# Kernel tuning notes

Hardware: AMD Instinct MI355X
Metric: run time of the kernel (lower is better)

The kernel has to match this reference:

```python
import jax, jax.numpy as jnp
import numpy as np

B, S, D_IN, D_EMB = 16, 8192, 256, 256
LEVELS = 8  # pywt default max level for db1 with signal length 256: log2(256)
INV_SQRT2 = np.float32(1.0 / np.sqrt(2.0))


def haar_wavedec_concat(x, levels):
    """Multi-level Haar (db1) DWT along last axis; returns coeffs concatenated
    in pywt order [cA_L, cD_L, ..., cD_1]. Assumes last dim = 2**levels,
    so 'symmetric' padding is a no-op (filter length 2, even lengths).
    pywt db1 convention: cA[k]=(x[2k]+x[2k+1])/sqrt2, cD[k]=(x[2k]-x[2k+1])/sqrt2.
    """
    details = []
    a = x
    for _ in range(levels):
        even = a[..., ::2]
        odd = a[..., 1::2]
        details.append((even - odd) * INV_SQRT2)
        a = (even + odd) * INV_SQRT2
    return jnp.concatenate([a] + details[::-1], axis=-1)


def setup_inputs() -> dict:
    key = jax.random.key(0)
    k_x, k_w, k_b = jax.random.split(key, 3)
    x = jax.random.normal(k_x, (B, S, D_IN), dtype=jnp.float32)
    # nn.Linear(input_dim, embed_dim): W is (embed_dim, input_dim)
    bound = np.float32(1.0 / np.sqrt(D_IN))
    W = jax.random.uniform(k_w, (D_EMB, D_IN), dtype=jnp.float32, minval=-bound, maxval=bound)
    b = jax.random.uniform(k_b, (D_EMB,), dtype=jnp.float32, minval=-bound, maxval=bound)
    return {"x": x, "W": W, "b": b}


def reference(x, W, b):
    coeffs = haar_wavedec_concat(x, LEVELS)  # (B, S, D_IN)
    # concatenated coeff length == D_IN exactly, so no pad/trim (matches original no-op branch)
    return jnp.einsum('bsd,ed->bse', coeffs, W) + b
```

## Files before the change

### kernel.cpp

```cpp
#include <hip/hip_runtime.h>
#include <hip/hip_bf16.h>

typedef short short8 __attribute__((ext_vector_type(8)));
typedef float f32x4 __attribute__((ext_vector_type(4)));

#define INV_SQRT2F 0.70710678118654752440f

__device__ __forceinline__ unsigned short f2bf(float f) {
  union { float f; unsigned u; } v; v.f = f;
  unsigned u = v.u;
  unsigned r = (u + 0x7FFFu + ((u >> 16) & 1u)) >> 16;
  return (unsigned short)r;
}

__global__ void haar_pack(const float* __restrict__ W, unsigned short* __restrict__ Wp) {
  __shared__ float cbuf[4][256];
  __shared__ float buf0[4][256];
  __shared__ float buf1[4][256];
  const int tid = threadIdx.x;
  const int w = tid >> 6, l = tid & 63;
  const int e = blockIdx.x * 4 + w;
  const float* row = W + e * 256;
  for (int k = l; k < 256; k += 64) cbuf[w][k] = row[k];
  __syncthreads();
  if (l == 0) buf0[w][0] = cbuf[w][0];
  __syncthreads();
  float* A = buf0[w];
  float* Bv = buf1[w];
  int len = 1;
  for (int s = 0; s < 8; ++s) {
    for (int k = l; k < len; k += 64) {
      float av = A[k], dv = cbuf[w][len + k];
      Bv[2 * k]     = (av + dv) * INV_SQRT2F;
      Bv[2 * k + 1] = (av - dv) * INV_SQRT2F;
    }
    __syncthreads();
    float* t = A; A = Bv; Bv = t;
    len <<= 1;
  }
  const int nblk = e >> 4, lr = e & 15;
  for (int k = l; k < 256; k += 64) {
    int kk = k >> 5, win = k & 31, lhi = win >> 3, j = win & 7;
    int lane = lhi * 16 + lr;
    Wp[(((nblk * 8 + kk) * 64 + lane) << 3) + j] = f2bf(A[k]);
  }
}

#define NTILES 16
#define BM 32

__global__ __launch_bounds__(512, 2) void wemb_gemm(
    const float* __restrict__ x, const unsigned short* __restrict__ Wp,
    const float* __restrict__ bias, float* __restrict__ out) {
  __shared__ char al[2][16384];
  const int tid = threadIdx.x;
  const int w = tid >> 6, lane = tid & 63;
  const int wm = w >> 2, wn = w & 3;
  const int lr = lane & 15, lhi = lane >> 4;

  short8 Bf[8][4];
#pragma unroll
  for (int kk = 0; kk < 8; ++kk)
#pragma unroll
    for (int n = 0; n < 4; ++n)
      Bf[kk][n] = *(const short8*)(Wp + ((((wn * 4 + n) * 8 + kk) * 64 + lane) << 3));

  float bv[4];
#pragma unroll
  for (int n = 0; n < 4; ++n) bv[n] = bias[wn * 64 + n * 16 + lr];

  const long tile0 = (long)blockIdx.x * NTILES;

  {
    const float4* src = (const float4*)(x + tile0 * (BM * 256));
#pragma unroll
    for (int i = 0; i < 4; ++i) {
      int f = i * 512 + tid;
      float4 v = src[f];
      int row = f >> 6, colb = (f & 63) * 8;
      ushort4 p; p.x = f2bf(v.x); p.y = f2bf(v.y); p.z = f2bf(v.z); p.w = f2bf(v.w);
      *(ushort4*)(al[0] + row * 512 + (colb ^ ((row & 7) << 4))) = p;
    }
  }
  __syncthreads();

#pragma unroll 1
  for (int it = 0; it < NTILES; ++it) {
    const long tt = tile0 + it;
    char* cur = al[it & 1];
    char* nxt = al[(it & 1) ^ 1];

    float4 pf[4];
    if (it < NTILES - 1) {
      const float4* src = (const float4*)(x + (tt + 1) * (BM * 256));
#pragma unroll
      for (int i = 0; i < 4; ++i) pf[i] = src[i * 512 + tid];
    }

    f32x4 acc[4];
#pragma unroll
    for (int n = 0; n < 4; ++n) acc[n] = (f32x4){0.f, 0.f, 0.f, 0.f};
#pragma unroll
    for (int kk = 0; kk < 8; ++kk) {
      const int arow = wm * 16 + lr;
      const int colb = (kk * 32 + lhi * 8) * 2;
      short8 a = *(const short8*)(cur + arow * 512 + (colb ^ ((arow & 7) << 4)));
#pragma unroll
      for (int n = 0; n < 4; ++n)
        acc[n] = __builtin_amdgcn_mfma_f32_16x16x32_bf16(a, Bf[kk][n], acc[n], 0, 0, 0);
    }

    {
      float* orow = out + (tt * BM + wm * 16 + lhi * 4) * 256;
#pragma unroll
      for (int n = 0; n < 4; ++n) {
        const int e = wn * 64 + n * 16 + lr;
#pragma unroll
        for (int r = 0; r < 4; ++r)
          __builtin_nontemporal_store(acc[n][r] + bv[n], orow + r * 256 + e);
      }
    }

    if (it < NTILES - 1) {
#pragma unroll
      for (int i = 0; i < 4; ++i) {
        int f = i * 512 + tid;
        int row = f >> 6, colb = (f & 63) * 8;
        ushort4 p; p.x = f2bf(pf[i].x); p.y = f2bf(pf[i].y); p.z = f2bf(pf[i].z); p.w = f2bf(pf[i].w);
        *(ushort4*)(nxt + row * 512 + (colb ^ ((row & 7) << 4))) = p;
      }
    }
    __syncthreads();
  }
}

extern "C" void kernel_launch(void* const* d_in, const int* in_sizes, int n_in,
                              void* d_out, int out_size, void* d_ws, size_t ws_size,
                              hipStream_t stream) {
  const float* x = (const float*)d_in[0];
  const float* W = (const float*)d_in[1];
  const float* b = (const float*)d_in[2];
  float* out = (float*)d_out;
  unsigned short* Wp = (unsigned short*)d_ws;

  haar_pack<<<64, 256, 0, stream>>>(W, Wp);

  const int grid = (out_size / 256) / (BM * NTILES);
  wemb_gemm<<<grid, 512, 0, stream>>>(x, Wp, b, out);
}
```

Baseline: 64.91 us.

## Deepen x prefetch to two tiles ahead with unrolled ping-pong register buffers

```diff
diff --git a/kernel.cpp b/kernel.cpp
--- a/kernel.cpp
+++ b/kernel.cpp
@@ -49,7 +49,14 @@
 #define NTILES 16
 #define BM 32
 
-__global__ __launch_bounds__(512, 2) void wemb_gemm(
+#define BARRIER_LGKM() do { \
+    __builtin_amdgcn_sched_barrier(0); \
+    asm volatile("s_waitcnt lgkmcnt(0)" ::: "memory"); \
+    __builtin_amdgcn_s_barrier(); \
+    __builtin_amdgcn_sched_barrier(0); \
+  } while (0)
+
+__global__ __launch_bounds__(512, 1) void wemb_gemm(
     const float* __restrict__ x, const unsigned short* __restrict__ Wp,
     const float* __restrict__ bias, float* __restrict__ out) {
   __shared__ char al[2][16384];
@@ -64,74 +71,95 @@
 #pragma unroll
     for (int n = 0; n < 4; ++n)
       Bf[kk][n] = *(const short8*)(Wp + ((((wn * 4 + n) * 8 + kk) * 64 + lane) << 3));
+#pragma unroll
+  for (int kk = 0; kk < 8; ++kk)
+#pragma unroll
+    for (int n = 0; n < 4; ++n)
+      asm volatile("" : "+v"(Bf[kk][n]));
 
   float bv[4];
 #pragma unroll
   for (int n = 0; n < 4; ++n) bv[n] = bias[wn * 64 + n * 16 + lr];
 
   const long tile0 = (long)blockIdx.x * NTILES;
+  float4 pfA[4], pfB[4];
 
   {
-    const float4* src = (const float4*)(x + tile0 * (BM * 256));
+    const float4* s0 = (const float4*)(x + tile0 * (BM * 256));
+    float4 t0[4];
+#pragma unroll
+    for (int i = 0; i < 4; ++i) t0[i] = s0[i * 512 + tid];
+    const float4* s1 = (const float4*)(x + (tile0 + 1) * (BM * 256));
+#pragma unroll
+    for (int i = 0; i < 4; ++i) pfA[i] = s1[i * 512 + tid];
 #pragma unroll
     for (int i = 0; i < 4; ++i) {
       int f = i * 512 + tid;
-      float4 v = src[f];
       int row = f >> 6, colb = (f & 63) * 8;
-      ushort4 p; p.x = f2bf(v.x); p.y = f2bf(v.y); p.z = f2bf(v.z); p.w = f2bf(v.w);
+      ushort4 p;
+      p.x = __bfloat16_as_ushort(__float2bfloat16(t0[i].x));
+      p.y = __bfloat16_as_ushort(__float2bfloat16(t0[i].y));
+      p.z = __bfloat16_as_ushort(__float2bfloat16(t0[i].z));
+      p.w = __bfloat16_as_ushort(__float2bfloat16(t0[i].w));
       *(ushort4*)(al[0] + row * 512 + (colb ^ ((row & 7) << 4))) = p;
     }
   }
-  __syncthreads();
+  BARRIER_LGKM();
+
+#define STEP(IT, CUR, NXT, PFU, PFL)                                          \
+  {                                                                           \
+    const long tt = tile0 + (IT);                                             \
+    if ((IT) + 2 < NTILES) {                                                  \
+      const float4* src = (const float4*)(x + (tt + 2) * (BM * 256));         \
+      _Pragma("unroll")                                                       \
+      for (int i = 0; i < 4; ++i) PFL[i] = src[i * 512 + tid];                \
+    }                                                                         \
+    f32x4 acc[4];                                                             \
+    _Pragma("unroll")                                                         \
+    for (int n = 0; n < 4; ++n) acc[n] = (f32x4){0.f, 0.f, 0.f, 0.f};         \
+    _Pragma("unroll")                                                         \
+    for (int kk = 0; kk < 8; ++kk) {                                          \
+      const int arow = wm * 16 + lr;                                          \
+      const int colb = (kk * 32 + lhi * 8) * 2;                               \
+      short8 a = *(const short8*)((CUR) + arow * 512 +                        \
+                                  (colb ^ ((arow & 7) << 4)));                \
+      _Pragma("unroll")                                                       \
+      for (int n = 0; n < 4; ++n)                                             \
+        acc[n] = __builtin_amdgcn_mfma_f32_16x16x32_bf16(a, Bf[kk][n],        \
+                                                         acc[n], 0, 0, 0);    \
+    }                                                                         \
+    {                                                                         \
+      float* orow = out + (tt * BM + wm * 16 + lhi * 4) * 256;                \
+      _Pragma("unroll")                                                       \
+      for (int n = 0; n < 4; ++n) {                                           \
+        const int e = wn * 64 + n * 16 + lr;                                  \
+        _Pragma("unroll")                                                     \
+        for (int r = 0; r < 4; ++r) orow[r * 256 + e] = acc[n][r] + bv[n];    \
+      }                                                                       \
+    }                                                                         \
+    if ((IT) + 1 < NTILES) {                                                  \
+      _Pragma("unroll")                                                       \
+      for (int i = 0; i < 4; ++i) {                                           \
+        int f = i * 512 + tid;                                                \
+        int row = f >> 6, colb = (f & 63) * 8;                                \
+        ushort4 p;                                                            \
+        p.x = __bfloat16_as_ushort(__float2bfloat16(PFU[i].x));               \
+        p.y = __bfloat16_as_ushort(__float2bfloat16(PFU[i].y));               \
+        p.z = __bfloat16_as_ushort(__float2bfloat16(PFU[i].z));               \
+        p.w = __bfloat16_as_ushort(__float2bfloat16(PFU[i].w));               \
+        *(ushort4*)((NXT) + row * 512 + (colb ^ ((row & 7) << 4))) = p;       \
+      }                                                                       \
+      BARRIER_LGKM();                                                         \
+    }                                                                         \
+  }
 
 #pragma unroll 1
-  for (int it = 0; it < NTILES; ++it) {
-    const long tt = tile0 + it;
-    char* cur = al[it & 1];
-    char* nxt = al[(it & 1) ^ 1];
-
-    float4 pf[4];
-    if (it < NTILES - 1) {
-      const float4* src = (const float4*)(x + (tt + 1) * (BM * 256));
-#pragma unroll
-      for (int i = 0; i < 4; ++i) pf[i] = src[i * 512 + tid];
-    }
-
-    f32x4 acc[4];
-#pragma unroll
-    for (int n = 0; n < 4; ++n) acc[n] = (f32x4){0.f, 0.f, 0.f, 0.f};
-#pragma unroll
-    for (int kk = 0; kk < 8; ++kk) {
-      const int arow = wm * 16 + lr;
-      const int colb = (kk * 32 + lhi * 8) * 2;
-      short8 a = *(const short8*)(cur + arow * 512 + (colb ^ ((arow & 7) << 4)));
-#pragma unroll
-      for (int n = 0; n < 4; ++n)
-        acc[n] = __builtin_amdgcn_mfma_f32_16x16x32_bf16(a, Bf[kk][n], acc[n], 0, 0, 0);
-    }
-
-    {
-      float* orow = out + (tt * BM + wm * 16 + lhi * 4) * 256;
-#pragma unroll
-      for (int n = 0; n < 4; ++n) {
-        const int e = wn * 64 + n * 16 + lr;
-#pragma unroll
-        for (int r = 0; r < 4; ++r)
-          __builtin_nontemporal_store(acc[n][r] + bv[n], orow + r * 256 + e);
-      }
-    }
-
-    if (it < NTILES - 1) {
-#pragma unroll
-      for (int i = 0; i < 4; ++i) {
-        int f = i * 512 + tid;
-        int row = f >> 6, colb = (f & 63) * 8;
-        ushort4 p; p.x = f2bf(pf[i].x); p.y = f2bf(pf[i].y); p.z = f2bf(pf[i].z); p.w = f2bf(pf[i].w);
-        *(ushort4*)(nxt + row * 512 + (colb ^ ((row & 7) << 4))) = p;
-      }
-    }
-    __syncthreads();
+  for (int ip = 0; ip < NTILES / 2; ++ip) {
+    const int it0 = ip * 2;
+    STEP(it0,     al[0], al[1], pfA, pfB);
+    STEP(it0 + 1, al[1], al[0], pfB, pfA);
   }
+#undef STEP
 }
 
 extern "C" void kernel_launch(void* const* d_in, const int* in_sizes, int n_in,
```

Result: faster. 57.94 us (-10.7%).
